# Optimization experiments

Hardware: AMD Instinct MI355X
Metric: run time of the kernel (lower is better)

Reference implementation:

```python
import jax, jax.numpy as jnp
import numpy as np

BN_EPS = 1e-5


def binarize(x):
    # sign binarization with straight-through estimator (identity grad)
    return x + jax.lax.stop_gradient(jnp.sign(x) - x)


def conv2d(x, w, stride):
    # x: [N,C,H,W], w: [O,I,kh,kw], VALID padding (PyTorch default padding=0)
    return jax.lax.conv_general_dilated(
        x, w, window_strides=(stride, stride), padding='VALID',
        dimension_numbers=('NCHW', 'OIHW', 'NCHW'))


def batchnorm(x, gamma, beta, mean, var):
    inv = gamma / jnp.sqrt(var + BN_EPS)          # [C]
    return x * inv[None, :, None, None] + (beta - mean * inv)[None, :, None, None]


def setup_inputs() -> dict:
    key = jax.random.key(0)
    ks = jax.random.split(key, 20)
    B = 8192
    f32 = jnp.float32
    d = {
        'x': jax.random.normal(ks[0], (B, 1, 24, 54), f32),
        'conv1_w': jax.random.normal(ks[1], (32, 1, 3, 3), f32) * 0.3,
        'conv1_b': jax.random.normal(ks[2], (32,), f32) * 0.1,
        'bn1_gamma': 1.0 + 0.1 * jax.random.normal(ks[3], (32,), f32),
        'bn1_beta': 0.1 * jax.random.normal(ks[4], (32,), f32),
        'bn1_mean': 0.1 * jax.random.normal(ks[5], (32,), f32),
        'bn1_var': jax.random.uniform(ks[6], (32,), f32, 0.5, 1.5),
        'conv2_w': jax.random.normal(ks[7], (64, 32, 3, 3), f32) * 0.1,
        'conv2_b': jax.random.normal(ks[8], (64,), f32) * 0.1,
        'bn2_gamma': 1.0 + 0.1 * jax.random.normal(ks[9], (64,), f32),
        'bn2_beta': 0.1 * jax.random.normal(ks[10], (64,), f32),
        'bn2_mean': 0.1 * jax.random.normal(ks[11], (64,), f32),
        'bn2_var': jax.random.uniform(ks[12], (64,), f32, 0.5, 1.5),
        'lin_w': jax.random.normal(ks[13], (500, 3840), f32) * 0.02,
        'lin_b': jax.random.normal(ks[14], (500,), f32) * 0.1,
        'out_w': jax.random.normal(ks[15], (10, 500), f32) * 0.05,
        'out_b': jax.random.normal(ks[16], (10,), f32) * 0.1,
    }
    return d


def reference(x, conv1_w, conv1_b, bn1_gamma, bn1_beta, bn1_mean, bn1_var,
              conv2_w, conv2_b, bn2_gamma, bn2_beta, bn2_mean, bn2_var,
              lin_w, lin_b, out_w, out_b):
    # conv1: input channels (1) != 3 -> input binarized; weight binarized; float bias
    h = conv2d(binarize(x), binarize(conv1_w), 2) + conv1_b[None, :, None, None]
    h = jax.nn.relu(batchnorm(h, bn1_gamma, bn1_beta, bn1_mean, bn1_var))  # [B,32,11,26]
    # conv2: input channels (32) != 3 -> input binarized (values in {0,1} post-ReLU)
    h = conv2d(binarize(h), binarize(conv2_w), 2) + conv2_b[None, :, None, None]
    h = jax.nn.relu(batchnorm(h, bn2_gamma, bn2_beta, bn2_mean, bn2_var))  # [B,64,5,12]
    h = h.reshape(-1, 3840)
    # BinarizeLinear: in_features (3840, 500) != 784 -> input binarized
    h = jax.nn.relu(binarize(h) @ binarize(lin_w).T + lin_b[None, :])      # [B,500]
    y = binarize(h) @ binarize(out_w).T + out_b[None, :]                   # [B,10]
    return y
```

## Files before the change

kernel.cpp:

```cpp
#include <hip/hip_runtime.h>
#include <cstdint>

#define BN_EPS 1e-5f

static constexpr int NB = 8192;
static constexpr int JLIN = 500;

typedef int v4i  __attribute__((ext_vector_type(4)));
typedef int v16i __attribute__((ext_vector_type(16)));


__global__ __launch_bounds__(256) void pack_kernel(
    const float* __restrict__ conv1_w, const float* __restrict__ conv1_b,
    const float* __restrict__ conv2_w, const float* __restrict__ conv2_b,
    const float* __restrict__ lin_w, const float* __restrict__ lin_b,
    const float* __restrict__ out_w,
    const float* __restrict__ bn1_g, const float* __restrict__ bn1_b,
    const float* __restrict__ bn1_m, const float* __restrict__ bn1_v,
    const float* __restrict__ bn2_g, const float* __restrict__ bn2_b,
    const float* __restrict__ bn2_m, const float* __restrict__ bn2_v,
    uint4* __restrict__ wbfrag, uint32_t* __restrict__ cdat,
    uint32_t* __restrict__ lut, uint32_t* __restrict__ wout,
    int* __restrict__ Tlin, uint4* __restrict__ wcfrag)
{
    __shared__ float    s_c1w[288];
    __shared__ uint32_t s_wp[32];
    __shared__ float    s_inv1[32], s_sh1[32], s_b1[32];

    int tid = threadIdx.x;
    int b   = blockIdx.x;

    if (b < 512) {
        int e  = b * 256 + tid;
        int L  = e & 63;
        int kq = (e >> 6) & 127;
        int jt = e >> 13;
        int j  = jt * 32 + (L & 31);
        int h  = L >> 5;
        uint32_t dd[4] = {0u, 0u, 0u, 0u};
        if (j < JLIN) {
            int c  = kq >> 1, hi = kq & 1;
            int nb = (hi ? 28 : 32) - 16 * h;
            const float* src = lin_w + (size_t)j * 3840 + c * 60 + hi * 32 + 16 * h;
            #pragma unroll
            for (int i = 0; i < 16; ++i) {
                uint32_t byte = 0;
                if (i < nb) byte = (src[i] > 0.0f) ? 0x01u : 0xFFu;
                dd[i >> 2] |= byte << (8 * (i & 3));
            }
        }
        wbfrag[e] = make_uint4(dd[0], dd[1], dd[2], dd[3]);
        return;
    }

    if (b >= 520) {
        int e = (b - 520) * 256 + tid;
        if (e < 1152) {
            int t = e >> 7;
            int n = (e >> 6) & 1;
            int L = e & 63;
            int c = n * 32 + (L & 31);
            int hb = L >> 5;
            bool flip = (bn2_g[c] < 0.0f);
            uint32_t dd[4] = {0u, 0u, 0u, 0u};
            #pragma unroll
            for (int i = 0; i < 16; ++i) {
                int ic = 16 * hb + i;
                float w = conv2_w[c * 288 + ic * 9 + t];
                uint32_t byte = ((w > 0.0f) == flip) ? 0xFFu : 0x01u;
                dd[i >> 2] |= byte << (8 * (i & 3));
            }
            wcfrag[e] = make_uint4(dd[0], dd[1], dd[2], dd[3]);
        }
        return;
    }

    int mb = b - 512;
    if (mb < 2) {
        for (int i = tid; i < 288; i += 256) s_c1w[i] = conv1_w[i];
        __syncthreads();
        if (tid < 32) {
            uint32_t wp = 0;
            for (int t = 0; t < 9; ++t)
                wp |= (s_c1w[tid * 9 + t] < 0.0f ? 1u : 0u) << t;
            s_wp[tid] = wp;
            float inv = bn1_g[tid] / sqrtf(bn1_v[tid] + BN_EPS);
            s_inv1[tid] = inv;
            s_sh1[tid]  = bn1_b[tid] - bn1_m[tid] * inv;
            s_b1[tid]   = conv1_b[tid];
        }
        __syncthreads();
        uint32_t px = (uint32_t)(mb * 256 + tid);
        uint32_t word = 0;
        for (int c = 0; c < 32; ++c) {
            int d = 9 - 2 * __popc(px ^ s_wp[c]);
            float z = __fadd_rn((float)d, s_b1[c]);
            z = __fadd_rn(__fmul_rn(z, s_inv1[c]), s_sh1[c]);
            word |= (z > 0.0f ? 1u : 0u) << c;
        }
        lut[px] = word;
        return;
    }

    int idx = (mb - 2) * 256 + tid;
    if (idx < 576) {
        int c = idx / 9, tap = idx % 9;
        uint32_t w = 0;
        for (int ic = 0; ic < 32; ++ic)
            w |= (conv2_w[c * 288 + ic * 9 + tap] > 0.0f ? 1u : 0u) << ic;
        float inv = bn2_g[c] / sqrtf(bn2_v[c] + BN_EPS);
        if (inv < 0.0f) w = ~w;
        cdat[tap * 64 + c] = w;
    } else if (idx < 576 + 64) {
        int c = idx - 576;
        float inv = bn2_g[c] / sqrtf(bn2_v[c] + BN_EPS);
        float sh  = bn2_b[c] - bn2_m[c] * inv;
        float b2  = conv2_b[c];
        int T = 10000;
        for (int u = -300; u <= 300; ++u) {
            float v = (inv < 0.0f) ? (float)(-u) : (float)u;
            float z = __fadd_rn(__fmul_rn(__fadd_rn(v, b2), inv), sh);
            if (z > 0.0f) { T = u; break; }
        }
        cdat[576 + c] = (uint32_t)T;
    } else if (idx < 576 + 64 + 512) {
        int j = idx - (576 + 64);
        int T = 10000;
        if (j < JLIN) {
            float lb = lin_b[j];
            int base = (int)floorf(-lb) - 2;
            for (int u = base; u <= base + 5; ++u)
                if (__fadd_rn((float)u, lb) > 0.0f) { T = u; break; }
        }
        Tlin[j] = T;
    } else if (idx < 576 + 64 + 512 + 160) {
        int t = idx - (576 + 64 + 512);
        int j = t >> 4, k = t & 15;
        uint32_t w = 0;
        for (int bb = 0; bb < 32; ++bb) {
            int jj = k * 32 + bb;
            if (jj < JLIN) w |= (out_w[j * 500 + jj] > 0.0f ? 1u : 0u) << bb;
        }
        wout[t] = w;
    }
}

__global__ __launch_bounds__(256) void conv_kernel(
    const float* __restrict__ x,
    const uint32_t* __restrict__ cdat,
    const uint32_t* __restrict__ lut,
    const uint4* __restrict__ wcfrag,
    uint32_t* __restrict__ h2b)
{
    __shared__ __align__(16) uint8_t s_bytes[2 * 286 * 32];
    __shared__ uint32_t s_lut[512];
    __shared__ __align__(8) uint32_t s_flat[2][44];
    __shared__ uint64_t s_bal[2][2][2][16];

    int tid  = threadIdx.x;
    int lane = tid & 63;
    int wv   = tid >> 6;
    int s0   = blockIdx.x * 2;

    s_lut[tid]       = lut[tid];
    s_lut[tid + 256] = lut[tid + 256];

    {
        int psl = wv >> 1, ph = wv & 1;
        const float* xs = x + (size_t)(s0 + psl) * 1296;
        int it0 = ph * 11, it1 = ph ? 21 : 11;
        for (int it = it0; it < it1; ++it) {
            int f = it * 64 + lane;
            float v = (f < 1296) ? xs[f] : 1.0f;
            uint64_t mk = __ballot(v < 0.0f);
            if (lane == 0) *((uint64_t*)&s_flat[psl][2 * it]) = mk;
        }
    }
    __syncthreads();

    for (int i = tid; i < 2 * 286; i += 256) {
        int sl = i / 286, wnd = i - sl * 286;
        int oy = wnd / 26, ox = wnd - oy * 26;
        uint32_t pxb = 0;
        #pragma unroll
        for (int ky = 0; ky < 3; ++ky) {
            int bitpos = 54 * (2 * oy + ky) + 2 * ox;
            int d  = bitpos >> 5;
            int sh = bitpos & 31;
            uint64_t wp = (uint64_t)s_flat[sl][d] | ((uint64_t)s_flat[sl][d + 1] << 32);
            pxb |= (((uint32_t)(wp >> sh)) & 7u) << (3 * ky);
        }
        uint32_t w = s_lut[pxb];
        uint32_t dw[8];
        #pragma unroll
        for (int q = 0; q < 8; ++q)
            dw[q] = (((w >> (4 * q)) & 0xFu) * 0x204081u) & 0x01010101u;
        uint4* dst = (uint4*)(s_bytes + ((size_t)sl * 286 + wnd) * 32);
        dst[0] = make_uint4(dw[0], dw[1], dw[2], dw[3]);
        dst[1] = make_uint4(dw[4], dw[5], dw[6], dw[7]);
    }
    __syncthreads();

    {
        int sl = wv >> 1, rt = wv & 1;
        int p = rt * 32 + (lane & 31);
        if (p > 59) p = 59;
        int oy = p / 12, ox = p - 12 * oy;
        int hb = lane >> 5;
        const uint8_t* abase = s_bytes + ((size_t)sl * 286 + 52 * oy + 2 * ox) * 32 + 16 * hb;
        const uint4* bbase = wcfrag + lane;

        v16i acc0 = {};
        v16i acc1 = {};
        #pragma unroll
        for (int t = 0; t < 9; ++t) {
            const int koff = (t / 3) * 26 + (t % 3);
            uint4 av = *(const uint4*)(abase + koff * 32);
            v4i af = {(int)av.x, (int)av.y, (int)av.z, (int)av.w};
            uint4 b0 = bbase[t * 128];
            uint4 b1 = bbase[t * 128 + 64];
            v4i bf0 = {(int)b0.x, (int)b0.y, (int)b0.z, (int)b0.w};
            v4i bf1 = {(int)b1.x, (int)b1.y, (int)b1.z, (int)b1.w};
            acc0 = __builtin_amdgcn_mfma_i32_32x32x32_i8(af, bf0, acc0, 0, 0, 0);
            acc1 = __builtin_amdgcn_mfma_i32_32x32x32_i8(af, bf1, acc1, 0, 0, 0);
        }

        int T0 = (int)cdat[576 + (lane & 31)];
        int T1 = (int)cdat[576 + 32 + (lane & 31)];
        #pragma unroll
        for (int r = 0; r < 16; ++r) {
            uint64_t m0 = __ballot(acc0[r] >= T0);
            uint64_t m1 = __ballot(acc1[r] >= T1);
            if (lane == 0) {
                s_bal[sl][rt][0][r] = m0;
                s_bal[sl][rt][1][r] = m1;
            }
        }
    }
    __syncthreads();

    if (tid < 128) {
        int esl = tid >> 6, c = tid & 63;
        int n = c >> 5, cc = c & 31;
        uint32_t w0 = 0, w1 = 0;
        #pragma unroll 4
        for (int p = 0; p < 60; ++p) {
            int rt = p >> 5, row = p & 31;
            int hh = (row >> 2) & 1;
            int r  = (row & 3) | ((row >> 3) << 2);
            uint32_t bit = (uint32_t)((s_bal[esl][rt][n][r] >> (cc + 32 * hh)) & 1u);
            if (p < 32) w0 |= bit << p; else w1 |= bit << (p - 32);
        }
        *(uint2*)(h2b + (size_t)(s0 + esl) * 128 + 2 * c) = make_uint2(w0, w1);
    }
}

__global__ __launch_bounds__(256) void lin2_kernel(
    const uint32_t* __restrict__ h2b,
    const uint4* __restrict__ wbfrag,
    const int* __restrict__ Tlin,
    uint32_t* __restrict__ h3w)
{
    __shared__ uint8_t As[64 * 520];

    int tid  = threadIdx.x;
    int lane = tid & 63;
    int wv   = __builtin_amdgcn_readfirstlane((int)(tid >> 6));
    int sblk = blockIdx.x >> 2;
    int jgrp = blockIdx.x & 3;
    int jt   = jgrp * 4 + wv;
    int s0   = sblk * 64;

    int T = Tlin[jt * 32 + (lane & 31)];
    int row  = lane & 31;
    int half = lane >> 5;

    v16i acc0 = {};
    v16i acc1 = {};

    for (int chunk = 0; chunk < 8; ++chunk) {
        for (int e = tid; e < 1024; e += 256) {
            int sm = e >> 4, wl = e & 15;
            uint32_t w = h2b[(size_t)(s0 + sm) * 128 + chunk * 16 + wl];
            uint32_t dw[8];
            #pragma unroll
            for (int q = 0; q < 8; ++q)
                dw[q] = (((w >> (4 * q)) & 0xFu) * 0x204081u) & 0x01010101u;
            uint64_t* dst = (uint64_t*)(As + sm * 520 + wl * 32);
            dst[0] = (uint64_t)dw[0] | ((uint64_t)dw[1] << 32);
            dst[1] = (uint64_t)dw[2] | ((uint64_t)dw[3] << 32);
            dst[2] = (uint64_t)dw[4] | ((uint64_t)dw[5] << 32);
            dst[3] = (uint64_t)dw[6] | ((uint64_t)dw[7] << 32);
        }
        __syncthreads();

        const uint4* bsrc = wbfrag + ((size_t)jt * 128 + chunk * 16) * 64 + lane;
        #pragma unroll 4
        for (int kq = 0; kq < 16; ++kq) {
            uint4 bw = bsrc[kq * 64];
            v4i bf = {(int)bw.x, (int)bw.y, (int)bw.z, (int)bw.w};
            const uint8_t* ap = As + row * 520 + kq * 32 + half * 16;
            uint64_t lo0 = *(const uint64_t*)ap;
            uint64_t hi0 = *(const uint64_t*)(ap + 8);
            const uint8_t* aq = ap + 32 * 520;
            uint64_t lo1 = *(const uint64_t*)aq;
            uint64_t hi1 = *(const uint64_t*)(aq + 8);
            v4i a0 = {(int)(uint32_t)lo0, (int)(lo0 >> 32),
                      (int)(uint32_t)hi0, (int)(hi0 >> 32)};
            v4i a1 = {(int)(uint32_t)lo1, (int)(lo1 >> 32),
                      (int)(uint32_t)hi1, (int)(hi1 >> 32)};
            acc0 = __builtin_amdgcn_mfma_i32_32x32x32_i8(a0, bf, acc0, 0, 0, 0);
            acc1 = __builtin_amdgcn_mfma_i32_32x32x32_i8(a1, bf, acc1, 0, 0, 0);
        }
        __syncthreads();
    }

    #pragma unroll
    for (int r = 0; r < 16; ++r) {
        int row0 = (r & 3) + 8 * (r >> 2);
        uint64_t mk0 = __ballot(acc0[r] >= T);
        uint64_t mk1 = __ballot(acc1[r] >= T);
        if (lane == 0) {
            h3w[(size_t)(s0 + row0) * 16 + jt]          = (uint32_t)mk0;
            h3w[(size_t)(s0 + row0 + 4) * 16 + jt]      = (uint32_t)(mk0 >> 32);
            h3w[(size_t)(s0 + 32 + row0) * 16 + jt]     = (uint32_t)mk1;
            h3w[(size_t)(s0 + 32 + row0 + 4) * 16 + jt] = (uint32_t)(mk1 >> 32);
        }
    }
}

__global__ __launch_bounds__(256) void out_kernel(
    const uint32_t* __restrict__ h3w,
    const uint32_t* __restrict__ wout,
    const float* __restrict__ out_b,
    float* __restrict__ out)
{
    int s = blockIdx.x * 256 + threadIdx.x;
    const uint4* hp = (const uint4*)(h3w + (size_t)s * 16);
    uint4 q0 = hp[0], q1 = hp[1], q2 = hp[2], q3 = hp[3];
    uint32_t w[16] = {q0.x, q0.y, q0.z, q0.w, q1.x, q1.y, q1.z, q1.w,
                      q2.x, q2.y, q2.z, q2.w, q3.x, q3.y, q3.z, q3.w};
    int B = 0;
    #pragma unroll
    for (int k = 0; k < 16; ++k) B += __popc(w[k]);
    #pragma unroll
    for (int o = 0; o < 10; ++o) {
        int P = 0;
        #pragma unroll
        for (int k = 0; k < 16; ++k) P += __popc(w[k] & wout[o * 16 + k]);
        out[(size_t)s * 10 + o] = __fadd_rn((float)(2 * P - B), out_b[o]);
    }
}

extern "C" void kernel_launch(void* const* d_in, const int* in_sizes, int n_in,
                              void* d_out, int out_size, void* d_ws, size_t ws_size,
                              hipStream_t stream)
{
    const float* x       = (const float*)d_in[0];
    const float* conv1_w = (const float*)d_in[1];
    const float* conv1_b = (const float*)d_in[2];
    const float* bn1_g   = (const float*)d_in[3];
    const float* bn1_b   = (const float*)d_in[4];
    const float* bn1_m   = (const float*)d_in[5];
    const float* bn1_v   = (const float*)d_in[6];
    const float* conv2_w = (const float*)d_in[7];
    const float* conv2_b = (const float*)d_in[8];
    const float* bn2_g   = (const float*)d_in[9];
    const float* bn2_b   = (const float*)d_in[10];
    const float* bn2_m   = (const float*)d_in[11];
    const float* bn2_v   = (const float*)d_in[12];
    const float* lin_w   = (const float*)d_in[13];
    const float* lin_b   = (const float*)d_in[14];
    const float* out_w   = (const float*)d_in[15];
    const float* out_b   = (const float*)d_in[16];

    char* ws = (char*)d_ws;
    uint32_t* h2b    = (uint32_t*)(ws + 0);
    uint4*    wbfrag = (uint4*)   (ws + 4194304);
    uint32_t* h3w    = (uint32_t*)(ws + 6291456);
    uint32_t* cdat   = (uint32_t*)(ws + 6815744);
    uint32_t* lut    = (uint32_t*)(ws + 6818304);
    uint32_t* wout   = (uint32_t*)(ws + 6820352);
    int*      Tlin   = (int*)     (ws + 6820992);
    uint4*    wcfrag = (uint4*)   (ws + 6855808);

    pack_kernel<<<525, 256, 0, stream>>>(conv1_w, conv1_b, conv2_w, conv2_b,
                                         lin_w, lin_b, out_w,
                                         bn1_g, bn1_b, bn1_m, bn1_v,
                                         bn2_g, bn2_b, bn2_m, bn2_v,
                                         wbfrag, cdat, lut, wout, Tlin, wcfrag);
    conv_kernel<<<NB / 2, 256, 0, stream>>>(x, cdat, lut, wcfrag, h2b);
    lin2_kernel<<<512, 256, 0, stream>>>(h2b, wbfrag, Tlin, h3w);
    out_kernel<<<32, 256, 0, stream>>>(h3w, wout, out_b, (float*)d_out);
}
```

Baseline: 189.7 us.

## Restructure conv kernel to one sample per wavefront without block barriers

```diff
diff --git a/kernel.cpp b/kernel.cpp
--- a/kernel.cpp
+++ b/kernel.cpp
@@ -152,106 +152,122 @@
     const uint4* __restrict__ wcfrag,
     uint32_t* __restrict__ h2b)
 {
-    __shared__ __align__(16) uint8_t s_bytes[2 * 286 * 32];
     __shared__ uint32_t s_lut[512];
-    __shared__ __align__(8) uint32_t s_flat[2][44];
-    __shared__ uint64_t s_bal[2][2][2][16];
+    __shared__ __align__(8) uint32_t s_flat[4][44];
+    __shared__ uint32_t s_words[4][288];
+    __shared__ uint64_t s_bal[4][2][2][16];
 
     int tid  = threadIdx.x;
     int lane = tid & 63;
     int wv   = tid >> 6;
-    int s0   = blockIdx.x * 2;
+    int s    = blockIdx.x * 4 + wv;
 
     s_lut[tid]       = lut[tid];
     s_lut[tid + 256] = lut[tid + 256];
-
-    {
-        int psl = wv >> 1, ph = wv & 1;
-        const float* xs = x + (size_t)(s0 + psl) * 1296;
-        int it0 = ph * 11, it1 = ph ? 21 : 11;
-        for (int it = it0; it < it1; ++it) {
-            int f = it * 64 + lane;
-            float v = (f < 1296) ? xs[f] : 1.0f;
-            uint64_t mk = __ballot(v < 0.0f);
-            if (lane == 0) *((uint64_t*)&s_flat[psl][2 * it]) = mk;
-        }
-    }
     __syncthreads();
 
-    for (int i = tid; i < 2 * 286; i += 256) {
-        int sl = i / 286, wnd = i - sl * 286;
-        int oy = wnd / 26, ox = wnd - oy * 26;
-        uint32_t pxb = 0;
+    const float* xs = x + (size_t)s * 1296;
+    float xv[21];
+    #pragma unroll
+    for (int it = 0; it < 21; ++it) {
+        int f = it * 64 + lane;
+        xv[it] = (f < 1296) ? xs[f] : 1.0f;
+    }
+    #pragma unroll
+    for (int it = 0; it < 21; ++it) {
+        uint64_t mk = __ballot(xv[it] < 0.0f);
+        if (lane == 0) *(uint64_t*)&s_flat[wv][2 * it] = mk;
+    }
+    asm volatile("s_waitcnt lgkmcnt(0)" ::: "memory");
+    __builtin_amdgcn_sched_barrier(0);
+
+    #pragma unroll
+    for (int ii = 0; ii < 5; ++ii) {
+        int wnd = ii * 64 + lane;
+        if (wnd < 286) {
+            int oy = wnd / 26, ox = wnd - 26 * oy;
+            uint32_t pxb = 0;
+            #pragma unroll
+            for (int ky = 0; ky < 3; ++ky) {
+                int bitpos = 54 * (2 * oy + ky) + 2 * ox;
+                int d = bitpos >> 5, sh = bitpos & 31;
+                uint64_t wp = (uint64_t)s_flat[wv][d] |
+                              ((uint64_t)s_flat[wv][d + 1] << 32);
+                pxb |= (((uint32_t)(wp >> sh)) & 7u) << (3 * ky);
+            }
+            s_words[wv][wnd] = s_lut[pxb];
+        }
+    }
+    asm volatile("s_waitcnt lgkmcnt(0)" ::: "memory");
+    __builtin_amdgcn_sched_barrier(0);
+
+    int row32 = lane & 31;
+    int hb    = lane >> 5;
+    int sh_hb = 16 * hb;
+    int p1v   = 32 + row32; if (p1v > 59) p1v = 59;
+    int wb0, wb1;
+    { int oy = row32 / 12, ox = row32 - 12 * oy; wb0 = 52 * oy + 2 * ox; }
+    { int oy = p1v / 12,   ox = p1v - 12 * oy;   wb1 = 52 * oy + 2 * ox; }
+
+    v16i acc[2][2] = {};
+    #pragma unroll
+    for (int t = 0; t < 9; ++t) {
+        const int koff = (t / 3) * 26 + (t % 3);
+        uint4 b0 = wcfrag[t * 128 + lane];
+        uint4 b1 = wcfrag[t * 128 + 64 + lane];
+        v4i bf0 = {(int)b0.x, (int)b0.y, (int)b0.z, (int)b0.w};
+        v4i bf1 = {(int)b1.x, (int)b1.y, (int)b1.z, (int)b1.w};
         #pragma unroll
-        for (int ky = 0; ky < 3; ++ky) {
-            int bitpos = 54 * (2 * oy + ky) + 2 * ox;
-            int d  = bitpos >> 5;
-            int sh = bitpos & 31;
-            uint64_t wp = (uint64_t)s_flat[sl][d] | ((uint64_t)s_flat[sl][d + 1] << 32);
-            pxb |= (((uint32_t)(wp >> sh)) & 7u) << (3 * ky);
-        }
-        uint32_t w = s_lut[pxb];
-        uint32_t dw[8];
-        #pragma unroll
-        for (int q = 0; q < 8; ++q)
-            dw[q] = (((w >> (4 * q)) & 0xFu) * 0x204081u) & 0x01010101u;
-        uint4* dst = (uint4*)(s_bytes + ((size_t)sl * 286 + wnd) * 32);
-        dst[0] = make_uint4(dw[0], dw[1], dw[2], dw[3]);
-        dst[1] = make_uint4(dw[4], dw[5], dw[6], dw[7]);
-    }
-    __syncthreads();
-
-    {
-        int sl = wv >> 1, rt = wv & 1;
-        int p = rt * 32 + (lane & 31);
-        if (p > 59) p = 59;
-        int oy = p / 12, ox = p - 12 * oy;
-        int hb = lane >> 5;
-        const uint8_t* abase = s_bytes + ((size_t)sl * 286 + 52 * oy + 2 * ox) * 32 + 16 * hb;
-        const uint4* bbase = wcfrag + lane;
-
-        v16i acc0 = {};
-        v16i acc1 = {};
-        #pragma unroll
-        for (int t = 0; t < 9; ++t) {
-            const int koff = (t / 3) * 26 + (t % 3);
-            uint4 av = *(const uint4*)(abase + koff * 32);
-            v4i af = {(int)av.x, (int)av.y, (int)av.z, (int)av.w};
-            uint4 b0 = bbase[t * 128];
-            uint4 b1 = bbase[t * 128 + 64];
-            v4i bf0 = {(int)b0.x, (int)b0.y, (int)b0.z, (int)b0.w};
-            v4i bf1 = {(int)b1.x, (int)b1.y, (int)b1.z, (int)b1.w};
-            acc0 = __builtin_amdgcn_mfma_i32_32x32x32_i8(af, bf0, acc0, 0, 0, 0);
-            acc1 = __builtin_amdgcn_mfma_i32_32x32x32_i8(af, bf1, acc1, 0, 0, 0);
-        }
-
-        int T0 = (int)cdat[576 + (lane & 31)];
-        int T1 = (int)cdat[576 + 32 + (lane & 31)];
+        for (int rt = 0; rt < 2; ++rt) {
+            uint32_t w  = s_words[wv][(rt ? wb1 : wb0) + koff];
+            uint32_t hw = w >> sh_hb;
+            v4i af;
+            af[0] = (int)((((hw      ) & 0xFu) * 0x204081u) & 0x01010101u);
+            af[1] = (int)((((hw >> 4 ) & 0xFu) * 0x204081u) & 0x01010101u);
+            af[2] = (int)((((hw >> 8 ) & 0xFu) * 0x204081u) & 0x01010101u);
+            af[3] = (int)((((hw >> 12) & 0xFu) * 0x204081u) & 0x01010101u);
+            acc[rt][0] = __builtin_amdgcn_mfma_i32_32x32x32_i8(af, bf0, acc[rt][0], 0, 0, 0);
+            acc[rt][1] = __builtin_amdgcn_mfma_i32_32x32x32_i8(af, bf1, acc[rt][1], 0, 0, 0);
+        }
+    }
+
+    int T0 = (int)cdat[576 + row32];
+    int T1 = (int)cdat[576 + 32 + row32];
+    #pragma unroll
+    for (int rt = 0; rt < 2; ++rt) {
         #pragma unroll
         for (int r = 0; r < 16; ++r) {
-            uint64_t m0 = __ballot(acc0[r] >= T0);
-            uint64_t m1 = __ballot(acc1[r] >= T1);
+            uint64_t m0 = __ballot(acc[rt][0][r] >= T0);
+            uint64_t m1 = __ballot(acc[rt][1][r] >= T1);
             if (lane == 0) {
-                s_bal[sl][rt][0][r] = m0;
-                s_bal[sl][rt][1][r] = m1;
+                s_bal[wv][rt][0][r] = m0;
+                s_bal[wv][rt][1][r] = m1;
             }
         }
     }
-    __syncthreads();
-
-    if (tid < 128) {
-        int esl = tid >> 6, c = tid & 63;
-        int n = c >> 5, cc = c & 31;
+    asm volatile("s_waitcnt lgkmcnt(0)" ::: "memory");
+    __builtin_amdgcn_sched_barrier(0);
+
+    {
+        int n  = lane >> 5, cc = lane & 31;
         uint32_t w0 = 0, w1 = 0;
-        #pragma unroll 4
-        for (int p = 0; p < 60; ++p) {
-            int rt = p >> 5, row = p & 31;
-            int hh = (row >> 2) & 1;
-            int r  = (row & 3) | ((row >> 3) << 2);
-            uint32_t bit = (uint32_t)((s_bal[esl][rt][n][r] >> (cc + 32 * hh)) & 1u);
-            if (p < 32) w0 |= bit << p; else w1 |= bit << (p - 32);
-        }
-        *(uint2*)(h2b + (size_t)(s0 + esl) * 128 + 2 * c) = make_uint2(w0, w1);
+        #pragma unroll
+        for (int rt = 0; rt < 2; ++rt) {
+            #pragma unroll
+            for (int r = 0; r < 16; ++r) {
+                const int base = (r & 3) + 8 * (r >> 2);
+                uint64_t m = s_bal[wv][rt][n][r];
+                uint32_t b0 = (uint32_t)(m >> cc) & 1u;
+                uint32_t b1 = (uint32_t)(m >> (cc + 32)) & 1u;
+                const int p0 = rt * 32 + base;
+                const int p1 = p0 + 4;
+                if (p0 < 32) w0 |= b0 << p0; else w1 |= b0 << (p0 - 32);
+                if (p1 < 60) {
+                    if (p1 < 32) w0 |= b1 << p1; else w1 |= b1 << (p1 - 32);
+                }
+            }
+        }
+        *(uint2*)(h2b + (size_t)s * 128 + 2 * lane) = make_uint2(w0, w1);
     }
 }
 
@@ -389,7 +405,7 @@
                                          bn1_g, bn1_b, bn1_m, bn1_v,
                                          bn2_g, bn2_b, bn2_m, bn2_v,
                                          wbfrag, cdat, lut, wout, Tlin, wcfrag);
-    conv_kernel<<<NB / 2, 256, 0, stream>>>(x, cdat, lut, wcfrag, h2b);
+    conv_kernel<<<NB / 4, 256, 0, stream>>>(x, cdat, lut, wcfrag, h2b);
     lin2_kernel<<<512, 256, 0, stream>>>(h2b, wbfrag, Tlin, h3w);
     out_kernel<<<32, 256, 0, stream>>>(h3w, wout, out_b, (float*)d_out);
 }
```

Result: faster. 175.3 us (-7.6%).
